# Optimization experiments

Hardware: AMD Instinct MI355X
Metric: run time of the kernel (lower is better)

The kernel has to match this reference:

```python
import jax, jax.numpy as jnp
import numpy as np

N, E, C, Z = 20000, 320000, 64, 10
NLM, NB, P = 9, 8, 4          # (lmax=2 -> 9 lm comps), 8 Bessel, 4 contraction paths
RMAX, AVG = 5.0, 16.0         # radial cutoff, avg_num_neighbors
L_OF_LM = jnp.array([0, 1, 1, 1, 2, 2, 2, 2, 2])  # which l each lm component belongs to


def _sph_harm(u):
    """Component-normalized real spherical harmonics, lmax=2. u: [E,3] unit vectors."""
    x, y, z = u[:, 0], u[:, 1], u[:, 2]
    s3, s5, s15 = jnp.sqrt(3.0), jnp.sqrt(5.0), jnp.sqrt(15.0)
    return jnp.stack([
        jnp.ones_like(x),
        s3 * x, s3 * y, s3 * z,
        s15 * x * y, s15 * y * z, 0.5 * s5 * (3.0 * z * z - 1.0),
        s15 * x * z, 0.5 * s15 * (x * x - y * y),
    ], axis=-1)  # [E, 9]


def _forward(positions, atomic_indices, edge_index, W_embed, W_up,
             mlp_w1, mlp_w2, mlp_w3, mlp_w4, U3, U2, U1, Wc3, Wc2, Wc1, W_out):
    sender, receiver = edge_index[0], edge_index[1]
    # edge vectors / lengths (shifts == 0)
    vec = positions[receiver] - positions[sender]               # [E,3]
    r = jnp.sqrt(jnp.sum(vec * vec, axis=-1) + 1e-12)           # [E]
    Y = _sph_harm(vec / r[:, None])                             # [E,9]
    # Bessel radial basis * polynomial cutoff (p=6)
    n = jnp.arange(1, NB + 1, dtype=positions.dtype)
    bessel = jnp.sqrt(2.0 / RMAX) * jnp.sin(n[None, :] * jnp.pi * r[:, None] / RMAX) / r[:, None]
    u = jnp.clip(r / RMAX, 0.0, 1.0)
    p = 6.0
    fcut = 1.0 - 0.5 * (p + 1) * (p + 2) * u**6 + p * (p + 2) * u**7 - 0.5 * p * (p + 1) * u**8
    edge_feats = bessel * fcut[:, None]                         # [E,8]
    # per-edge tensor-product weights: SiLU MLP, no biases (MACE FullyConnectedNet)
    f = jax.nn.silu(edge_feats @ mlp_w1)
    f = jax.nn.silu(f @ mlp_w2)
    f = jax.nn.silu(f @ mlp_w3)
    tpw = (f @ mlp_w4).reshape(-1, 3, C)                        # [E, n_l=3, C]
    # node embedding (one-hot linear) + linear_up, e3nn 1/sqrt(fan_in) norm
    h = W_embed[atomic_indices] / jnp.sqrt(jnp.asarray(Z, positions.dtype))  # [N,C]
    h = (h @ W_up) / jnp.sqrt(jnp.asarray(C, positions.dtype))               # [N,C]
    # channelwise tensor product 64x0e (x) (0e+1o+2e): gather-TP
    w_lm = tpw[:, L_OF_LM, :]                                   # [E,9,C]
    mji = h[sender][:, :, None] * jnp.swapaxes(w_lm, 1, 2) * Y[:, None, :]  # [E,C,9]
    # scatter-sum messages to receivers
    message = jax.ops.segment_sum(mji, receiver, num_segments=N) / AVG       # [N,C,9]
    x = message  # reshape() output: [N, C, lm]
    # symmetric product contraction (correlation=3), element-dependent weights
    W3n, W2n, W1n = Wc3[atomic_indices], Wc2[atomic_indices], Wc1[atomic_indices]  # [N,P,C]
    out = jnp.einsum('ijkp,npc,nci->ncjk', U3, W3n, x)          # [N,C,9,9]
    c2 = jnp.einsum('jkp,npc->ncjk', U2, W2n) + out
    out = jnp.einsum('ncjk,nck->ncj', c2, x)                    # [N,C,9]
    c1 = jnp.einsum('jp,npc->ncj', U1, W1n) + out
    out = jnp.einsum('ncj,ncj->nc', c1, x)                      # [N,C] invariant output
    return (out @ W_out) / jnp.sqrt(jnp.asarray(C, positions.dtype))


def setup_inputs() -> dict:
    key = jax.random.key(0)
    ks = jax.random.split(key, 16)
    return {
        'positions': jax.random.normal(ks[0], (N, 3), jnp.float32),
        'atomic_indices': jax.random.randint(ks[1], (N,), 0, Z),
        'edge_index': jax.random.randint(ks[2], (2, E), 0, N),
        'W_embed': jax.random.normal(ks[3], (Z, C), jnp.float32),
        'W_up': jax.random.normal(ks[4], (C, C), jnp.float32),
        'mlp_w1': jax.random.normal(ks[5], (NB, 64), jnp.float32) / np.sqrt(NB),
        'mlp_w2': jax.random.normal(ks[6], (64, 64), jnp.float32) / 8.0,
        'mlp_w3': jax.random.normal(ks[7], (64, 64), jnp.float32) / 8.0,
        'mlp_w4': jax.random.normal(ks[8], (64, 3 * C), jnp.float32) / 8.0,
        'U3': jax.random.normal(ks[9], (NLM, NLM, NLM, P), jnp.float32) * 0.1,
        'U2': jax.random.normal(ks[10], (NLM, NLM, P), jnp.float32) * 0.1,
        'U1': jax.random.normal(ks[11], (NLM, P), jnp.float32) * 0.1,
        'Wc3': jax.random.normal(ks[12], (Z, P, C), jnp.float32) * 0.1,
        'Wc2': jax.random.normal(ks[13], (Z, P, C), jnp.float32) * 0.1,
        'Wc1': jax.random.normal(ks[14], (Z, P, C), jnp.float32) * 0.1,
        'W_out': jax.random.normal(ks[15], (C, C), jnp.float32),
    }


def reference(positions, atomic_indices, edge_index, W_embed, W_up,
              mlp_w1, mlp_w2, mlp_w3, mlp_w4, U3, U2, U1, Wc3, Wc2, Wc1, W_out):
    return _forward(positions, atomic_indices, edge_index, W_embed, W_up,
                    mlp_w1, mlp_w2, mlp_w3, mlp_w4, U3, U2, U1, Wc3, Wc2, Wc1, W_out)
```

## Files before the change

### kernel.cpp

```cpp
#include <hip/hip_runtime.h>
#include <hip/hip_bf16.h>

typedef unsigned short u16;
typedef unsigned int u32;
typedef __attribute__((ext_vector_type(8))) short bf16x8;
typedef __attribute__((ext_vector_type(4))) float f32x4;

#define NN 20000
#define NE 320000

#define WP_H     256
#define WP_U1    3072
#define WP_U2    3328
#define WP_U3    4096
#define WP_CUR   7168
#define WP_POSF  87168
#define WP_WB    407168
#define WP_EL16  452224

__device__ __forceinline__ float bf2f(u16 u){ return __uint_as_float(((u32)u) << 16); }
__device__ __forceinline__ u16 f2bf(float f){
  u32 u = __float_as_uint(f);
  u32 r = (u + 0x7fffu + ((u >> 16) & 1u)) >> 16;
  return (u16)r;
}
__device__ __forceinline__ u16 f2bfa(float f){
  return (u16)((__float_as_uint(f) + 0x8000u) >> 16);
}
__device__ __forceinline__ u32 pk2bf(float a, float b){
  __hip_bfloat162 h = __float22bfloat162_rn(make_float2(a, b));
  return *(u32*)&h;
}
__device__ __forceinline__ float silu_f(float v){
  return v * __builtin_amdgcn_rcpf(1.0f + __expf(-v));
}
__device__ __forceinline__ float ldf(const void* p, int i, int bf){
  return bf ? bf2f(((const u16*)p)[i]) : ((const float*)p)[i];
}
__device__ __forceinline__ f32x4 mfma16(bf16x8 a, bf16x8 b, f32x4 c){
  return __builtin_amdgcn_mfma_f32_16x16x32_bf16(a, b, c, 0, 0, 0);
}

#define SOFT_FENCE() do { \
  __builtin_amdgcn_wave_barrier(); \
  asm volatile("" ::: "memory"); \
  __builtin_amdgcn_wave_barrier(); \
} while (0)

__device__ __forceinline__ int sniff_wave(const u32* wu, int lane){
  u32 w = wu[lane];
  u32 e = (w >> 7) & 0xFFu;
  unsigned long long m = __ballot(e >= 0x60u && e <= 0x86u);
  return (__popcll(m) > 37) ? 1 : 0;
}

extern "C" __global__ __launch_bounds__(256)
void k_prep_pad(const void* __restrict__ We, const void* __restrict__ Wu,
                const void* __restrict__ U3, const void* __restrict__ U2, const void* __restrict__ U1,
                const void* __restrict__ w1, const void* __restrict__ w2,
                const void* __restrict__ w3, const void* __restrict__ w4,
                const void* __restrict__ pos, const int* __restrict__ eidx,
                float* __restrict__ Hws, float* __restrict__ U3ws,
                float* __restrict__ U2ws, float* __restrict__ U1ws,
                u16* __restrict__ wbws, float4* __restrict__ posf,
                int* __restrict__ cur, u16* __restrict__ el16)
{
  int tid = threadIdx.x;
  int b = blockIdx.x;
  int bf = sniff_wave((const u32*)Wu, tid & 63);

  {
    int e = b*256 + tid;
    int r = eidx[NE + e];
    int s = eidx[e];
    int slot = atomicAdd(&cur[r], 1);
    if (slot < 64) el16[(r << 6) + slot] = (u16)s;
  }

  if (b == 0){
    for (int t = tid; t < 36; t += 256) U1ws[t] = ldf(U1, t, bf);
    for (int t = tid; t < 45; t += 256){
      int j = 0, rem = t;
      for (;;){ int cnt = 9 - j; if (rem < cnt) break; rem -= cnt; ++j; }
      int k = j + rem;
      for (int p = 0; p < 4; ++p){
        float v = ldf(U2, (j*9 + k)*4 + p, bf);
        if (k > j) v += ldf(U2, (k*9 + j)*4 + p, bf);
        U2ws[t*4 + p] = v;
      }
    }
    for (int t = tid; t < 165; t += 256){
      int i = 0, rem = t;
      for (;;){ int m = 9 - i; int cnt = m*(m+1)/2; if (rem < cnt) break; rem -= cnt; ++i; }
      int j = i;
      for (;;){ int cnt = 9 - j; if (rem < cnt) break; rem -= cnt; ++j; }
      int k = j + rem;
      int pm[6][3] = {{i,j,k},{i,k,j},{j,i,k},{j,k,i},{k,i,j},{k,j,i}};
      float acc[4] = {0,0,0,0};
      for (int m = 0; m < 6; ++m){
        bool dup = false;
        for (int mm = 0; mm < m; ++mm)
          if (pm[mm][0]==pm[m][0] && pm[mm][1]==pm[m][1] && pm[mm][2]==pm[m][2]) dup = true;
        if (!dup){
          int base = ((pm[m][0]*9 + pm[m][1])*9 + pm[m][2])*4;
          for (int p = 0; p < 4; ++p) acc[p] += ldf(U3, base + p, bf);
        }
      }
      for (int p = 0; p < 4; ++p) U3ws[t*4 + p] = acc[p];
    }
  } else if (b <= 88){
    int idx = (b - 1)*256 + tid;
    int f = idx >> 9;
    int L = (idx >> 3) & 63;
    int j = idx & 7;
    int kl = ((L >> 4) << 3) + j;
    int n16 = L & 15;
    float v;
    if (f < 4){
      v = (kl < 8) ? ldf(w1, kl*64 + (f*16 + n16), bf) : 0.f;
    } else if (f < 12){
      int g = f - 4; int t = g >> 1, q = g & 1;
      v = ldf(w2, (q*32 + kl)*64 + (t*16 + n16), bf);
    } else if (f < 20){
      int g = f - 12; int t = g >> 1, q = g & 1;
      v = ldf(w3, (q*32 + kl)*64 + (t*16 + n16), bf);
    } else {
      int g = f - 20; int lt = g >> 1, q = g & 1;
      int l = lt >> 2, ct = lt & 3;
      v = ldf(w4, (q*32 + kl)*192 + (l*64 + ct*16 + n16), bf);
    }
    wbws[idx] = f2bf(v);
  } else if (b <= 167){
    int i = (b - 89)*256 + tid;
    if (i < NN){
      float4 v;
      v.x = ldf(pos, 3*i+0, bf); v.y = ldf(pos, 3*i+1, bf); v.z = ldf(pos, 3*i+2, bf); v.w = 0.f;
      posf[i] = v;
    }
  } else if (b <= 177){
    int z = b - 168;
    int c = tid;
    if (c < 64){
      float s = 0.f;
      for (int k = 0; k < 64; ++k) s += ldf(We, z*64 + k, bf) * ldf(Wu, k*64 + c, bf);
      Hws[z*64 + c] = s * 0.0395284708f;
    }
  }
}

__device__ __forceinline__ void edge_geom(float4 pr, float4 ps, float* ef, float* Y)
{
  float vx = pr.x - ps.x, vy = pr.y - ps.y, vz = pr.z - ps.z;
  float r2 = vx*vx + vy*vy + vz*vz + 1e-12f;
  float rinv = rsqrtf(r2);
  float r = r2 * rinv;
  float ux = vx*rinv, uy = vy*rinv, uz = vz*rinv;
  const float s3 = 1.7320508076f, s5 = 2.2360679775f, s15 = 3.8729833462f;
  Y[0] = 1.0f;
  Y[1] = s3*ux; Y[2] = s3*uy; Y[3] = s3*uz;
  Y[4] = s15*ux*uy; Y[5] = s15*uy*uz;
  Y[6] = 0.5f*s5*(3.0f*uz*uz - 1.0f);
  Y[7] = s15*ux*uz;
  Y[8] = 0.5f*s15*(ux*ux - uy*uy);
  float u = r * 0.2f; u = fminf(u, 1.0f);
  float u2 = u*u, u4 = u2*u2, u6 = u4*u2, u7 = u6*u, u8 = u7*u;
  float fc = 1.0f - 28.0f*u6 + 48.0f*u7 - 21.0f*u8;
  float c0 = 0.63245553203f * fc * rinv;
  float w = 0.62831853072f * r;
  #pragma unroll
  for (int k = 0; k < 8; ++k) ef[k] = c0 * __sinf(w * (float)(k + 1));
}

extern "C" __global__ __launch_bounds__(256, 3)
void k_main(const int* __restrict__ atom,
            const void* __restrict__ Wu,
            const void* __restrict__ Wc3, const void* __restrict__ Wc2, const void* __restrict__ Wc1,
            const void* __restrict__ Woutg,
            const float* __restrict__ Hws, const float* __restrict__ U3ws,
            const float* __restrict__ U2ws, const float* __restrict__ U1ws,
            const float4* __restrict__ posf,
            const int* __restrict__ deg, const u16* __restrict__ el16,
            const u16* __restrict__ wbws, void* __restrict__ outp)
{
  __shared__ __align__(16) u16   wb[12288];
  __shared__ __align__(16) u16   act[4][1024];
  __shared__ __align__(16) u16   efb[4][64][8];
  __shared__ __align__(16) u16   Yc8[4][64][8];

  int tid = threadIdx.x;
  int wv = tid >> 6;
  int lane = tid & 63;
  int bf = sniff_wave((const u32*)Wu, lane);

  for (int t = tid; t < 6144; t += 256) ((u32*)wb)[t] = ((const u32*)wbws)[5120 + t];
  __syncthreads();

  int c0 = lane & 15;
  int qd = lane >> 4;
  int n = blockIdx.x * 4 + wv;
  int cnt = min(deg[n], 64);
  float4 pr = posf[n];

  u16* A = &act[wv][0];
  int swr = qd << 4;
  int srd = (c0 >> 2) << 4;

  bf16x8 w1p[4], w2p[8], w3p[8];
  #pragma unroll
  for (int t = 0; t < 4; ++t) w1p[t] = *(const bf16x8*)&wbws[t*512 + lane*8];
  #pragma unroll
  for (int g = 0; g < 8; ++g) w2p[g] = *(const bf16x8*)&wbws[(4+g)*512 + lane*8];
  #pragma unroll
  for (int g = 0; g < 8; ++g) w3p[g] = *(const bf16x8*)&wbws[(12+g)*512 + lane*8];

  int lmap = (c0 == 0) ? 0 : (c0 < 4) ? 1 : 2;
  u32 msk1 = (lmap == 1) ? 0xFFFFFFFFu : 0u;
  u32 msk2 = (lmap == 2) ? 0xFFFFFFFFu : 0u;

  const f32x4 zero4 = {0.f, 0.f, 0.f, 0.f};
  f32x4 XD[4];
  #pragma unroll
  for (int t = 0; t < 4; ++t) XD[t] = zero4;

  int prow = ((qd >> 1) << 4) + c0;
  int pcol = (qd & 1) << 2;
  int ntile = (cnt + 15) >> 4;

  int zreg;
  {
    bool valid = lane < cnt;
    int sid = valid ? (int)el16[(n << 6) + lane] : n;
    float4 ps = posf[sid];
    zreg = valid ? atom[sid] : 0;
    float ef[8], Y[9];
    edge_geom(pr, ps, ef, Y);
    if (!valid){
      #pragma unroll
      for (int k = 0; k < 8; ++k) ef[k] = 0.f;
      #pragma unroll
      for (int m = 0; m < 9; ++m) Y[m] = 0.f;
    }
    uint4 pk;
    pk.x = pk2bf(ef[0], ef[1]);
    pk.y = pk2bf(ef[2], ef[3]);
    pk.z = pk2bf(ef[4], ef[5]);
    pk.w = pk2bf(ef[6], ef[7]);
    *(uint4*)&efb[wv][lane][0] = pk;
    uint4 yp;
    yp.x = pk2bf(Y[1], Y[2]);
    yp.y = pk2bf(Y[3], Y[4]);
    yp.z = pk2bf(Y[5], Y[6]);
    yp.w = pk2bf(Y[7], Y[8]);
    *(uint4*)&Yc8[wv][lane][0] = yp;
  }
  SOFT_FENCE();

  #pragma unroll 1
  for (int t = 0; t < ntile; ++t){
    f32x4 dd[4];

    bf16x8 aF = {0,0,0,0,0,0,0,0};
    if (lane < 16) aF = *(const bf16x8*)&efb[wv][t*16 + lane][0];
    #pragma unroll
    for (int t2 = 0; t2 < 4; ++t2) dd[t2] = mfma16(aF, w1p[t2], zero4);
    #pragma unroll
    for (int t2 = 0; t2 < 4; ++t2)
      #pragma unroll
      for (int r = 0; r < 4; ++r)
        A[(((qd*4 + r) << 6) + c0 + (t2 << 4)) ^ swr] = f2bfa(silu_f(dd[t2][r]));
    SOFT_FENCE();

    bf16x8 a0 = *(const bf16x8*)&A[((c0 << 6) + (qd << 3)) ^ srd];
    bf16x8 a1 = *(const bf16x8*)&A[((c0 << 6) + 32 + (qd << 3)) ^ srd];
    #pragma unroll
    for (int t2 = 0; t2 < 4; ++t2)
      dd[t2] = mfma16(a1, w2p[t2*2+1], mfma16(a0, w2p[t2*2+0], zero4));
    #pragma unroll
    for (int t2 = 0; t2 < 4; ++t2)
      #pragma unroll
      for (int r = 0; r < 4; ++r)
        A[(((qd*4 + r) << 6) + c0 + (t2 << 4)) ^ swr] = f2bfa(silu_f(dd[t2][r]));
    SOFT_FENCE();

    a0 = *(const bf16x8*)&A[((c0 << 6) + (qd << 3)) ^ srd];
    a1 = *(const bf16x8*)&A[((c0 << 6) + 32 + (qd << 3)) ^ srd];
    #pragma unroll
    for (int t2 = 0; t2 < 4; ++t2)
      dd[t2] = mfma16(a1, w3p[t2*2+1], mfma16(a0, w3p[t2*2+0], zero4));
    #pragma unroll
    for (int t2 = 0; t2 < 4; ++t2)
      #pragma unroll
      for (int r = 0; r < 4; ++r)
        A[(((qd*4 + r) << 6) + c0 + (t2 << 4)) ^ swr] = f2bfa(silu_f(dd[t2][r]));
    SOFT_FENCE();

    a0 = *(const bf16x8*)&A[((c0 << 6) + (qd << 3)) ^ srd];
    a1 = *(const bf16x8*)&A[((c0 << 6) + 32 + (qd << 3)) ^ srd];

    u32 yd0 = 0, yd1 = 0, yd2 = 0, yd3 = 0;
    if (lane < 32 && c0 >= 1 && c0 <= 8){
      const u16* yr = &Yc8[wv][t*16 + ((lane >> 4) << 3)][c0 - 1];
      yd0 = (u32)yr[0*8] | ((u32)yr[1*8] << 16);
      yd1 = (u32)yr[2*8] | ((u32)yr[3*8] << 16);
      yd2 = (u32)yr[4*8] | ((u32)yr[5*8] << 16);
      yd3 = (u32)yr[6*8] | ((u32)yr[7*8] << 16);
    }
    u32 b00 = 0, b01 = 0, b02 = 0, b03 = 0;
    if (lane < 32 && c0 == 0){
      int k0 = t*16 + ((lane >> 4) << 3);
      b00 = ((k0+0 < cnt) ? 0x3F80u : 0u) | ((k0+1 < cnt) ? 0x3F800000u : 0u);
      b01 = ((k0+2 < cnt) ? 0x3F80u : 0u) | ((k0+3 < cnt) ? 0x3F800000u : 0u);
      b02 = ((k0+4 < cnt) ? 0x3F80u : 0u) | ((k0+5 < cnt) ? 0x3F800000u : 0u);
      b03 = ((k0+6 < cnt) ? 0x3F80u : 0u) | ((k0+7 < cnt) ? 0x3F800000u : 0u);
    }
    bf16x8 B0, B1, B2;
    { uint4 t0 = {b00, b01, b02, b03};
      uint4 t1 = {yd0 & msk1, yd1 & msk1, yd2 & msk1, yd3 & msk1};
      uint4 t2 = {yd0 & msk2, yd1 & msk2, yd2 & msk2, yd3 & msk2};
      B0 = *(bf16x8*)&t0; B1 = *(bf16x8*)&t1; B2 = *(bf16x8*)&t2; }

    float hv[4][4];
    #pragma unroll
    for (int r = 0; r < 4; ++r){
      int z_e = __shfl(zreg, t*16 + qd*4 + r);
      #pragma unroll
      for (int ct = 0; ct < 4; ++ct) hv[r][ct] = Hws[z_e*64 + ct*16 + c0];
    }

    u16* PF = A;
    #pragma unroll
    for (int l = 0; l < 3; ++l){
      #pragma unroll
      for (int ct = 0; ct < 4; ++ct){
        int f = (l*4 + ct)*2;
        bf16x8 b0 = *(const bf16x8*)&wb[f*512 + lane*8];
        bf16x8 b1 = *(const bf16x8*)&wb[(f+1)*512 + lane*8];
        dd[ct] = mfma16(a1, b1, mfma16(a0, b0, zero4));
      }
      #pragma unroll
      for (int ct = 0; ct < 4; ++ct){
        uint2 pk2;
        pk2.x = pk2bf(hv[0][ct] * dd[ct][0], hv[1][ct] * dd[ct][1]);
        pk2.y = pk2bf(hv[2][ct] * dd[ct][2], hv[3][ct] * dd[ct][3]);
        *(uint2*)&PF[ct*256 + prow*8 + pcol] = pk2;
      }
      SOFT_FENCE();
      bf16x8 Bl = (l == 0) ? B0 : (l == 1) ? B1 : B2;
      #pragma unroll
      for (int ct = 0; ct < 4; ++ct){
        bf16x8 aP = {0,0,0,0,0,0,0,0};
        if (lane < 32) aP = *(const bf16x8*)&PF[ct*256 + lane*8];
        XD[ct] = mfma16(aP, Bl, XD[ct]);
      }
      SOFT_FENCE();
    }
  }

  float* Xf8 = (float*)A;
  float* X8f = (float*)&efb[wv][0][0];
  SOFT_FENCE();
  #pragma unroll
  for (int ct = 0; ct < 4; ++ct)
    #pragma unroll
    for (int r = 0; r < 4; ++r){
      int c = ct*16 + qd*4 + r;
      if (c0 < 8)       Xf8[c*8 + c0] = XD[ct][r];
      else if (c0 == 8) X8f[c]        = XD[ct][r];
    }
  SOFT_FENCE();
  float X[9];
  {
    const float4* xr = (const float4*)&Xf8[lane*8];
    float4 xa = xr[0], xb = xr[1];
    X[0]=xa.x; X[1]=xa.y; X[2]=xa.z; X[3]=xa.w;
    X[4]=xb.x; X[5]=xb.y; X[6]=xb.z; X[7]=xb.w;
    X[8]=X8f[lane];
  }
  #pragma unroll
  for (int m = 0; m < 9; ++m) X[m] *= 0.0625f;

  const float4* U1g = (const float4*)U1ws;
  const float4* U2g = (const float4*)U2ws;
  const float4* U3g = (const float4*)U3ws;
  float s1a[4] = {0,0,0,0}, s2a[4] = {0,0,0,0}, s3a[4] = {0,0,0,0};
  #pragma unroll
  for (int j = 0; j < 9; ++j){
    float4 u = U1g[j];
    s1a[0] += u.x*X[j]; s1a[1] += u.y*X[j]; s1a[2] += u.z*X[j]; s1a[3] += u.w*X[j];
  }
  {
    int t2i = 0;
    #pragma unroll
    for (int j = 0; j < 9; ++j)
      #pragma unroll
      for (int k = j; k < 9; ++k){
        float m = X[j]*X[k];
        float4 u = U2g[t2i]; ++t2i;
        s2a[0] += u.x*m; s2a[1] += u.y*m; s2a[2] += u.z*m; s2a[3] += u.w*m;
      }
  }
  {
    int t3i = 0;
    #pragma unroll
    for (int i = 0; i < 9; ++i)
      #pragma unroll
      for (int j = i; j < 9; ++j){
        float mij = X[i]*X[j];
        #pragma unroll
        for (int k = j; k < 9; ++k){
          float m = mij*X[k];
          float4 u = U3g[t3i]; ++t3i;
          s3a[0] += u.x*m; s3a[1] += u.y*m; s3a[2] += u.z*m; s3a[3] += u.w*m;
        }
      }
  }

  int zn = atom[n];
  float outval = 0.f;
  #pragma unroll
  for (int p = 0; p < 4; ++p){
    int b = (zn*4 + p)*64 + lane;
    outval += ldf(Wc1, b, bf)*s1a[p] + ldf(Wc2, b, bf)*s2a[p] + ldf(Wc3, b, bf)*s3a[p];
  }

  float* xchg = (float*)A;
  SOFT_FENCE();
  xchg[lane] = outval;
  SOFT_FENCE();
  float acc = 0.f;
  const float4* pb = (const float4*)xchg;
  if (bf){
    const u16* wg = (const u16*)Woutg;
    #pragma unroll
    for (int cb = 0; cb < 16; ++cb){
      float4 p = pb[cb];
      acc += p.x*bf2f(wg[(4*cb+0)*64 + lane]) + p.y*bf2f(wg[(4*cb+1)*64 + lane])
           + p.z*bf2f(wg[(4*cb+2)*64 + lane]) + p.w*bf2f(wg[(4*cb+3)*64 + lane]);
    }
  } else {
    const float* wg = (const float*)Woutg;
    #pragma unroll
    for (int cb = 0; cb < 16; ++cb){
      float4 p = pb[cb];
      acc += p.x*wg[(4*cb+0)*64 + lane] + p.y*wg[(4*cb+1)*64 + lane]
           + p.z*wg[(4*cb+2)*64 + lane] + p.w*wg[(4*cb+3)*64 + lane];
    }
  }
  acc *= 0.125f;
  if (bf) ((u16*)outp)[n*64 + lane] = f2bf(acc);
  else    ((float*)outp)[n*64 + lane] = acc;
}

extern "C" void kernel_launch(void* const* d_in, const int* in_sizes, int n_in,
                              void* d_out, int out_size, void* d_ws, size_t ws_size,
                              hipStream_t stream)
{
  const void* pos  = d_in[0];
  const int* atom  = (const int*)d_in[1];
  const int* eidx  = (const int*)d_in[2];
  const void* We   = d_in[3];
  const void* Wu   = d_in[4];
  const void* w1g  = d_in[5];
  const void* w2g  = d_in[6];
  const void* w3g  = d_in[7];
  const void* w4g  = d_in[8];
  const void* U3   = d_in[9];
  const void* U2   = d_in[10];
  const void* U1   = d_in[11];
  const void* Wc3  = d_in[12];
  const void* Wc2  = d_in[13];
  const void* Wc1  = d_in[14];
  const void* Wout = d_in[15];

  char* ws = (char*)d_ws;
  float*  Hws   = (float*)(ws + WP_H);
  float*  U1ws  = (float*)(ws + WP_U1);
  float*  U2ws  = (float*)(ws + WP_U2);
  float*  U3ws  = (float*)(ws + WP_U3);
  int*    cur   = (int*)(ws + WP_CUR);
  float4* posf  = (float4*)(ws + WP_POSF);
  u16*    wbws  = (u16*)(ws + WP_WB);
  u16*    el16  = (u16*)(ws + WP_EL16);

  (void)hipMemsetAsync(ws + WP_CUR, 0, 80000, stream);
  k_prep_pad<<<1250, 256, 0, stream>>>(We, Wu, U3, U2, U1, w1g, w2g, w3g, w4g, pos, eidx,
                                       Hws, U3ws, U2ws, U1ws, wbws, posf, cur, el16);
  k_main<<<5000, 256, 0, stream>>>(atom, Wu, Wc3, Wc2, Wc1, Wout,
                                   Hws, U3ws, U2ws, U1ws, posf,
                                   cur, el16, wbws, d_out);
}
```

Before: 300.4 us.

## Stream MLP weights per tile, overlap weight staging with edge geometry

The first two MLP layers' weight fragments are no longer held in registers for the whole kernel. They are reloaded from global memory inside each edge tile, and an opaque scalar offset keeps the compiler from hoisting them back out, which cuts register pressure. The shared weight copy now uses 16-byte loads and is issued together with the neighbor/position gathers and edge geometry, with one block barrier afterwards, so the copy latency overlaps useful work. The symmetric-contraction accumulators are rewritten as vector float4 multiply-adds. The trade-off is extra global/L2 loads of weights on every tile.

```diff
diff --git a/kernel.cpp b/kernel.cpp
--- a/kernel.cpp
+++ b/kernel.cpp
@@ -192,46 +192,27 @@
   int lane = tid & 63;
   int bf = sniff_wave((const u32*)Wu, lane);
 
-  for (int t = tid; t < 6144; t += 256) ((u32*)wb)[t] = ((const u32*)wbws)[5120 + t];
-  __syncthreads();
-
   int c0 = lane & 15;
   int qd = lane >> 4;
   int n = blockIdx.x * 4 + wv;
+
   int cnt = min(deg[n], 64);
+  int el  = (int)el16[(n << 6) + lane];
   float4 pr = posf[n];
 
-  u16* A = &act[wv][0];
-  int swr = qd << 4;
-  int srd = (c0 >> 2) << 4;
-
-  bf16x8 w1p[4], w2p[8], w3p[8];
-  #pragma unroll
-  for (int t = 0; t < 4; ++t) w1p[t] = *(const bf16x8*)&wbws[t*512 + lane*8];
-  #pragma unroll
-  for (int g = 0; g < 8; ++g) w2p[g] = *(const bf16x8*)&wbws[(4+g)*512 + lane*8];
+  for (int t = tid; t < 1536; t += 256)
+    ((uint4*)wb)[t] = ((const uint4*)wbws)[1280 + t];
+
+  bool valid = lane < cnt;
+  int sid = valid ? el : n;
+  float4 ps = posf[sid];
+  int zreg = valid ? atom[sid] : 0;
+
+  bf16x8 w3p[8];
   #pragma unroll
   for (int g = 0; g < 8; ++g) w3p[g] = *(const bf16x8*)&wbws[(12+g)*512 + lane*8];
 
-  int lmap = (c0 == 0) ? 0 : (c0 < 4) ? 1 : 2;
-  u32 msk1 = (lmap == 1) ? 0xFFFFFFFFu : 0u;
-  u32 msk2 = (lmap == 2) ? 0xFFFFFFFFu : 0u;
-
-  const f32x4 zero4 = {0.f, 0.f, 0.f, 0.f};
-  f32x4 XD[4];
-  #pragma unroll
-  for (int t = 0; t < 4; ++t) XD[t] = zero4;
-
-  int prow = ((qd >> 1) << 4) + c0;
-  int pcol = (qd & 1) << 2;
-  int ntile = (cnt + 15) >> 4;
-
-  int zreg;
   {
-    bool valid = lane < cnt;
-    int sid = valid ? (int)el16[(n << 6) + lane] : n;
-    float4 ps = posf[sid];
-    zreg = valid ? atom[sid] : 0;
     float ef[8], Y[9];
     edge_geom(pr, ps, ef, Y);
     if (!valid){
@@ -253,16 +234,39 @@
     yp.w = pk2bf(Y[7], Y[8]);
     *(uint4*)&Yc8[wv][lane][0] = yp;
   }
-  SOFT_FENCE();
+  __syncthreads();
+
+  u16* A = &act[wv][0];
+  int swr = qd << 4;
+  int srd = (c0 >> 2) << 4;
+
+  int lmap = (c0 == 0) ? 0 : (c0 < 4) ? 1 : 2;
+  u32 msk1 = (lmap == 1) ? 0xFFFFFFFFu : 0u;
+  u32 msk2 = (lmap == 2) ? 0xFFFFFFFFu : 0u;
+
+  const f32x4 zero4 = {0.f, 0.f, 0.f, 0.f};
+  f32x4 XD[4];
+  #pragma unroll
+  for (int t = 0; t < 4; ++t) XD[t] = zero4;
+
+  int prow = ((qd >> 1) << 4) + c0;
+  int pcol = (qd & 1) << 2;
+  int ntile = (cnt + 15) >> 4;
+
+  u32 zofs = 0;
 
   #pragma unroll 1
   for (int t = 0; t < ntile; ++t){
+    asm volatile("" : "+s"(zofs));
     f32x4 dd[4];
 
     bf16x8 aF = {0,0,0,0,0,0,0,0};
     if (lane < 16) aF = *(const bf16x8*)&efb[wv][t*16 + lane][0];
     #pragma unroll
-    for (int t2 = 0; t2 < 4; ++t2) dd[t2] = mfma16(aF, w1p[t2], zero4);
+    for (int t2 = 0; t2 < 4; ++t2){
+      bf16x8 w1f = *(const bf16x8*)&wbws[zofs + t2*512 + lane*8];
+      dd[t2] = mfma16(aF, w1f, zero4);
+    }
     #pragma unroll
     for (int t2 = 0; t2 < 4; ++t2)
       #pragma unroll
@@ -273,8 +277,11 @@
     bf16x8 a0 = *(const bf16x8*)&A[((c0 << 6) + (qd << 3)) ^ srd];
     bf16x8 a1 = *(const bf16x8*)&A[((c0 << 6) + 32 + (qd << 3)) ^ srd];
     #pragma unroll
-    for (int t2 = 0; t2 < 4; ++t2)
-      dd[t2] = mfma16(a1, w2p[t2*2+1], mfma16(a0, w2p[t2*2+0], zero4));
+    for (int t2 = 0; t2 < 4; ++t2){
+      bf16x8 w2a = *(const bf16x8*)&wbws[zofs + (4 + t2*2)*512 + lane*8];
+      bf16x8 w2b = *(const bf16x8*)&wbws[zofs + (5 + t2*2)*512 + lane*8];
+      dd[t2] = mfma16(a1, w2b, mfma16(a0, w2a, zero4));
+    }
     #pragma unroll
     for (int t2 = 0; t2 < 4; ++t2)
       #pragma unroll
@@ -379,15 +386,12 @@
   #pragma unroll
   for (int m = 0; m < 9; ++m) X[m] *= 0.0625f;
 
-  const float4* U1g = (const float4*)U1ws;
-  const float4* U2g = (const float4*)U2ws;
-  const float4* U3g = (const float4*)U3ws;
-  float s1a[4] = {0,0,0,0}, s2a[4] = {0,0,0,0}, s3a[4] = {0,0,0,0};
-  #pragma unroll
-  for (int j = 0; j < 9; ++j){
-    float4 u = U1g[j];
-    s1a[0] += u.x*X[j]; s1a[1] += u.y*X[j]; s1a[2] += u.z*X[j]; s1a[3] += u.w*X[j];
-  }
+  const f32x4* U1g = (const f32x4*)U1ws;
+  const f32x4* U2g = (const f32x4*)U2ws;
+  const f32x4* U3g = (const f32x4*)U3ws;
+  f32x4 s1 = zero4, s2 = zero4, s3 = zero4;
+  #pragma unroll
+  for (int j = 0; j < 9; ++j) s1 += U1g[j] * X[j];
   {
     int t2i = 0;
     #pragma unroll
@@ -395,8 +399,7 @@
       #pragma unroll
       for (int k = j; k < 9; ++k){
         float m = X[j]*X[k];
-        float4 u = U2g[t2i]; ++t2i;
-        s2a[0] += u.x*m; s2a[1] += u.y*m; s2a[2] += u.z*m; s2a[3] += u.w*m;
+        s2 += U2g[t2i] * m; ++t2i;
       }
   }
   {
@@ -408,9 +411,7 @@
         float mij = X[i]*X[j];
         #pragma unroll
         for (int k = j; k < 9; ++k){
-          float m = mij*X[k];
-          float4 u = U3g[t3i]; ++t3i;
-          s3a[0] += u.x*m; s3a[1] += u.y*m; s3a[2] += u.z*m; s3a[3] += u.w*m;
+          s3 += U3g[t3i] * (mij*X[k]); ++t3i;
         }
       }
   }
@@ -420,7 +421,7 @@
   #pragma unroll
   for (int p = 0; p < 4; ++p){
     int b = (zn*4 + p)*64 + lane;
-    outval += ldf(Wc1, b, bf)*s1a[p] + ldf(Wc2, b, bf)*s2a[p] + ldf(Wc3, b, bf)*s3a[p];
+    outval += ldf(Wc1, b, bf)*s1[p] + ldf(Wc2, b, bf)*s2[p] + ldf(Wc3, b, bf)*s3[p];
   }
 
   float* xchg = (float*)A;
```

Measured after the change: 278.1 us. 7.4% less time.
